# Performance work log

Hardware: AMD Instinct MI355X
Metric: run time of the kernel (lower is better)

The kernel has to match this reference:

```python
import jax, jax.numpy as jnp
import numpy as np

N, H, C, K, D = 16384, 16, 192, 43, 2
SIGMA = 1.0   # radius == sigma in Block
BN_EPS = 1e-5


def setup_inputs() -> dict:
    key = jax.random.key(0)
    ks = jax.random.split(key, 8)
    coord = jax.random.uniform(ks[0], (N, 3), dtype=jnp.float32)
    feat = jax.random.normal(ks[1], (N, C), dtype=jnp.float32)
    ref_idx = jax.random.randint(ks[2], (N, H), 0, N)
    # kernel point dispositions, within radius
    kp = jax.random.normal(ks[3], (K, 3), dtype=jnp.float32) * (0.3 * SIGMA)
    W1 = jax.random.normal(ks[4], (D, C, C), dtype=jnp.float32) / np.sqrt(C)
    Wk = jax.random.normal(ks[5], (D, K, C), dtype=jnp.float32) / np.sqrt(K * H)
    W3 = jax.random.normal(ks[6], (D, C, C), dtype=jnp.float32) / np.sqrt(C)
    ones = jnp.ones((D, C), jnp.float32)
    zeros = jnp.zeros((D, C), jnp.float32)
    return {
        "coord": coord, "feat": feat, "ref_idx": ref_idx, "kp": kp,
        "W1": W1, "Wk": Wk, "W3": W3,
        "g1": ones, "b1": zeros, "g2": ones, "b2": zeros, "g3": ones, "b3": zeros,
    }


def _bn(x, g, b):
    # PointBatchNorm on [N, C]: batch statistics over the point axis
    m = jnp.mean(x, axis=0)
    v = jnp.var(x, axis=0)
    return (x - m) * jax.lax.rsqrt(v + BN_EPS) * g + b


def reference(coord, feat, ref_idx, kp, W1, Wk, W3, g1, b1, g2, b2, g3, b3):
    # --- KP influence, shared across blocks (same coords / neighbor table) ---
    nb = coord[ref_idx] - coord[:, None, :]                       # [N,H,3] relative neighbor coords
    d2 = (jnp.sum(nb * nb, -1)[..., None]
          + jnp.sum(kp * kp, -1)[None, None, :]
          - 2.0 * jnp.einsum('nhd,kd->nhk', nb, kp))              # [N,H,K]
    d = jnp.sqrt(jnp.maximum(d2, 0.0))
    infl = jnp.maximum(1.0 - d / SIGMA, 0.0)                      # linear influence [N,H,K]

    relu = jax.nn.relu
    depth = W1.shape[0]
    for i in range(depth):
        identity = feat
        h = relu(_bn(feat @ W1[i], g1[i], b1[i]))                 # fc1 + BN + ReLU
        # KPConvD: depthwise kernel-point conv
        A = jnp.einsum('nhk,kc->nhc', infl, Wk[i])                # influence-projected depthwise weights
        h = jnp.einsum('nhc,nhc->nc', h[ref_idx], A)              # gather + weighted aggregate
        h = relu(_bn(h, g2[i], b2[i]))
        h = _bn(h @ W3[i], g3[i], b3[i])                          # fc3 + BN
        feat = relu(identity + h)                                 # skip + ReLU
    return feat
```

## Files before the change

### kernel.cpp

```cpp
#include <hip/hip_runtime.h>

#define N_PTS 16384
#define NH 16
#define NC 192
#define NK 43
#define ND 2
#define BN_EPS 1e-5f
#define NB 16
#define STSTRIDE (NB * 384)

typedef __attribute__((ext_vector_type(8))) short bf16x8;
typedef __attribute__((ext_vector_type(4))) float f32x4;

static __device__ __forceinline__ short f2bf(float f) {
    union { float f; unsigned u; } x; x.f = f;
    unsigned r = x.u + (0x7fffu + ((x.u >> 16) & 1u));
    return (short)(r >> 16);
}
static __device__ __forceinline__ float bf2f(short s) {
    union { unsigned u; float f; } x; x.u = ((unsigned)(unsigned short)s) << 16;
    return x.f;
}

static __device__ __forceinline__ void bank_sum(const float* __restrict__ acc, int c,
                                                float& s, float& q) {
    s = 0.f; q = 0.f;
#pragma unroll
    for (int k = 0; k < NB; ++k) {
        s += acc[k * 384 + c];
        q += acc[k * 384 + 192 + c];
    }
}

__global__ __launch_bounds__(64) void k_wfrag(const float* __restrict__ W1,
                                              const float* __restrict__ Wk,
                                              const float* __restrict__ W3,
                                              short* __restrict__ Wb,
                                              float* __restrict__ stacc) {
    for (int z = blockIdx.x * 64 + threadIdx.x; z < 6 * STSTRIDE; z += 336 * 64)
        stacc[z] = 0.f;

    int b = blockIdx.x;
    int d = b / 168, r = b % 168;
    const float* src; short* dst; int kb, Ks, tile;
    if (r < 72)      { src = W1 + d * NC * NC; dst = Wb + d * 86016;         kb = 6; Ks = NC; tile = r; }
    else if (r < 96) { src = Wk + d * NK * NC; dst = Wb + d * 86016 + 36864; kb = 2; Ks = NK; tile = r - 72; }
    else             { src = W3 + d * NC * NC; dst = Wb + d * 86016 + 49152; kb = 6; Ks = NC; tile = r - 96; }
    int nt = tile / kb, ks = tile % kb;
    int lane = threadIdx.x, quad = lane >> 4, cl = lane & 15;
    bf16x8 vv;
#pragma unroll
    for (int j = 0; j < 8; ++j) {
        int k = ks * 32 + quad * 8 + j;
        vv[j] = (k < Ks) ? f2bf(src[k * NC + nt * 16 + cl]) : (short)0;
    }
    *(bf16x8*)(dst + ((nt * kb + ks) * 64 + lane) * 8) = vv;
}

__global__ __launch_bounds__(256, 1) void k_gemm1(const float* __restrict__ feat,
                                                  const short* __restrict__ T2prev,
                                                  const float* __restrict__ st3acc,
                                                  const float* __restrict__ g3,
                                                  const float* __restrict__ b3,
                                                  short* __restrict__ X1,
                                                  const short* __restrict__ W1b,
                                                  short* __restrict__ T,
                                                  float* __restrict__ st1acc) {
    __shared__ float red[4][384];
    __shared__ float pa_s[192], ps_s[192];
    const int tid = threadIdx.x;
    const int wave = tid >> 6, lane = tid & 63;
    const int quad = lane >> 4, cl = lane & 15;
    const int r0 = blockIdx.x * 64 + wave * 16;
    const int row = r0 + cl;

    if (T2prev) {
        if (tid < 192) {
            float s, q; bank_sum(st3acc, tid, s, q);
            float m = s * (1.f / N_PTS);
            float v = q * (1.f / N_PTS) - m * m;
            float a = rsqrtf(v + BN_EPS) * g3[tid];
            pa_s[tid] = a;
            ps_s[tid] = b3[tid] - m * a;
        }
        __syncthreads();
    }

    float4 fa[6][2];
    bf16x8 t2v[6];
#pragma unroll
    for (int ks = 0; ks < 6; ++ks) {
        const float* ap = feat + row * NC + ks * 32 + quad * 8;
        fa[ks][0] = *(const float4*)ap;
        fa[ks][1] = *(const float4*)(ap + 4);
    }
    if (T2prev) {
#pragma unroll
        for (int ks = 0; ks < 6; ++ks)
            t2v[ks] = *(const bf16x8*)(T2prev + row * NC + ks * 32 + quad * 8);
    }

    f32x4 acc[12];
#pragma unroll
    for (int nt = 0; nt < 12; ++nt) acc[nt] = (f32x4){0.f, 0.f, 0.f, 0.f};

#pragma unroll
    for (int ks = 0; ks < 6; ++ks) {
        const int k0 = ks * 32 + quad * 8;
        float x[8] = {fa[ks][0].x, fa[ks][0].y, fa[ks][0].z, fa[ks][0].w,
                      fa[ks][1].x, fa[ks][1].y, fa[ks][1].z, fa[ks][1].w};
        if (T2prev) {
#pragma unroll
            for (int j = 0; j < 8; ++j)
                x[j] = fmaxf(x[j] + fmaf(pa_s[k0 + j], bf2f(t2v[ks][j]), ps_s[k0 + j]), 0.f);
        }
        bf16x8 af;
#pragma unroll
        for (int j = 0; j < 8; ++j) af[j] = f2bf(x[j]);
        if (T2prev) *(bf16x8*)(X1 + row * NC + k0) = af;
#pragma unroll
        for (int nt = 0; nt < 12; ++nt) {
            bf16x8 bf = *(const bf16x8*)(W1b + ((nt * 6 + ks) * 64 + lane) * 8);
            acc[nt] = __builtin_amdgcn_mfma_f32_16x16x32_bf16(af, bf, acc[nt], 0, 0, 0);
        }
    }
#pragma unroll
    for (int nt = 0; nt < 12; ++nt) {
        int c = nt * 16 + cl;
        float s = 0.f, sq = 0.f;
#pragma unroll
        for (int r = 0; r < 4; ++r) {
            float v = acc[nt][r];
            T[(r0 + quad * 4 + r) * NC + c] = f2bf(v);
            s += v; sq = fmaf(v, v, sq);
        }
        s += __shfl_xor(s, 16); s += __shfl_xor(s, 32);
        sq += __shfl_xor(sq, 16); sq += __shfl_xor(sq, 32);
        if (quad == 0) { red[wave][c] = s; red[wave][192 + c] = sq; }
    }
    __syncthreads();
    {
        float* dst = st1acc + (blockIdx.x & (NB - 1)) * 384;
        for (int t = tid; t < 384; t += 256)
            atomicAdd(&dst[t], red[0][t] + red[1][t] + red[2][t] + red[3][t]);
    }
}

__global__ __launch_bounds__(512) void k_kpconv(const float* __restrict__ coord,
                                                const int* __restrict__ ridx,
                                                const float* __restrict__ kp,
                                                const short* __restrict__ Wkb,
                                                const short* __restrict__ T,
                                                const float* __restrict__ st1acc,
                                                const float* __restrict__ g1,
                                                const float* __restrict__ b1,
                                                short* __restrict__ U,
                                                float* __restrict__ st2acc) {
    __shared__ __align__(16) short wk_s[12288];
    __shared__ __align__(16) float4 kp_s[64];
    __shared__ float a1s[192], s1s[192];
    __shared__ float red[8][384];

    const int tid = threadIdx.x;
    {
        const float4* src = (const float4*)Wkb;
        float4* dst = (float4*)wk_s;
        for (int j = tid; j < 1536; j += 512) dst[j] = src[j];
        if (tid < 64) {
            bool ok = tid < NK;
            float x = ok ? kp[tid * 3 + 0] : 1e9f;
            float y = ok ? kp[tid * 3 + 1] : 1e9f;
            float z = ok ? kp[tid * 3 + 2] : 1e9f;
            kp_s[tid] = (float4){x, y, z, fmaf(x, x, fmaf(y, y, z * z))};
        }
        if (tid < 192) {
            float s, q; bank_sum(st1acc, tid, s, q);
            float m = s * (1.f / N_PTS);
            float v = q * (1.f / N_PTS) - m * m;
            float a = rsqrtf(v + BN_EPS) * g1[tid];
            a1s[tid] = a;
            s1s[tid] = b1[tid] - m * a;
        }
    }
    __syncthreads();

    const int wave = tid >> 6, lane = tid & 63;
    const int quad = lane >> 4, cl = lane & 15;
    const int n = blockIdx.x * 8 + wave;

    int idh = 0; float nbx = 0.f, nby = 0.f, nbz = 0.f;
    if (lane < NH) {
        idh = ridx[n * NH + lane];
        float cx = coord[n * 3 + 0], cy = coord[n * 3 + 1], cz = coord[n * 3 + 2];
        nbx = coord[idh * 3 + 0] - cx;
        nby = coord[idh * 3 + 1] - cy;
        nbz = coord[idh * 3 + 2] - cz;
    }
    const float nx = __shfl(nbx, cl), ny = __shfl(nby, cl), nz = __shfl(nbz, cl);
    int rowb[4];
#pragma unroll
    for (int r = 0; r < 4; ++r) rowb[r] = __shfl(idh, quad * 4 + r) * NC;

    unsigned short xv[12][4];
    const unsigned short* Tu = (const unsigned short*)T;
#pragma unroll
    for (int nt = 0; nt < 12; ++nt)
#pragma unroll
        for (int r = 0; r < 4; ++r)
            xv[nt][r] = Tu[rowb[r] + nt * 16 + cl];

    const float nb2 = fmaf(nx, nx, fmaf(ny, ny, nz * nz));
    const float m2x = -2.f * nx, m2y = -2.f * ny, m2z = -2.f * nz;
    bf16x8 af[2];
#pragma unroll
    for (int ks = 0; ks < 2; ++ks) {
#pragma unroll
        for (int j = 0; j < 8; ++j) {
            int k = ks * 32 + quad * 8 + j;
            float4 kpv = kp_s[k];
            float t = nb2 + kpv.w;
            t = fmaf(m2x, kpv.x, t);
            t = fmaf(m2y, kpv.y, t);
            t = fmaf(m2z, kpv.z, t);
            float d = sqrtf(fmaxf(t, 0.f));
            af[ks][j] = f2bf(fmaxf(1.f - d, 0.f));
        }
    }

    f32x4 acc[12];
#pragma unroll
    for (int nt = 0; nt < 12; ++nt) {
        bf16x8 b0 = *(const bf16x8*)(wk_s + ((nt * 2 + 0) * 64 + lane) * 8);
        bf16x8 b1v = *(const bf16x8*)(wk_s + ((nt * 2 + 1) * 64 + lane) * 8);
        f32x4 z = (f32x4){0.f, 0.f, 0.f, 0.f};
        z = __builtin_amdgcn_mfma_f32_16x16x32_bf16(af[0], b0, z, 0, 0, 0);
        acc[nt] = __builtin_amdgcn_mfma_f32_16x16x32_bf16(af[1], b1v, z, 0, 0, 0);
    }

#pragma unroll
    for (int nt = 0; nt < 12; ++nt) {
        const float a1c = a1s[nt * 16 + cl], s1c = s1s[nt * 16 + cl];
        float u = 0.f;
#pragma unroll
        for (int r = 0; r < 4; ++r) {
            float t = bf2f((short)xv[nt][r]);
            float x = fmaxf(fmaf(a1c, t, s1c), 0.f);
            u = fmaf(acc[nt][r], x, u);
        }
        u += __shfl_xor(u, 16);
        u += __shfl_xor(u, 32);
        if (quad == 0) {
            U[n * NC + nt * 16 + cl] = f2bf(u);
            red[wave][nt * 16 + cl] = u;
            red[wave][192 + nt * 16 + cl] = u * u;
        }
    }

    __syncthreads();
    if (tid < 384) {
        float S = 0.f;
#pragma unroll
        for (int w = 0; w < 8; ++w) S += red[w][tid];
        atomicAdd(&st2acc[(blockIdx.x & (NB - 1)) * 384 + tid], S);
    }
}

__global__ __launch_bounds__(256, 1) void k_gemm3(const short* __restrict__ U,
                                                  const float* __restrict__ st2acc,
                                                  const float* __restrict__ g2,
                                                  const float* __restrict__ b2,
                                                  const short* __restrict__ W3b,
                                                  short* __restrict__ T2,
                                                  float* __restrict__ st3acc) {
    __shared__ float red[4][384];
    __shared__ float a2s[192], s2s[192];
    const int tid = threadIdx.x;
    const int wave = tid >> 6, lane = tid & 63;
    const int quad = lane >> 4, cl = lane & 15;
    const int r0 = blockIdx.x * 64 + wave * 16;
    const int row = r0 + cl;

    if (tid < 192) {
        float s, q; bank_sum(st2acc, tid, s, q);
        float m = s * (1.f / N_PTS);
        float v = q * (1.f / N_PTS) - m * m;
        float a = rsqrtf(v + BN_EPS) * g2[tid];
        a2s[tid] = a;
        s2s[tid] = b2[tid] - m * a;
    }
    __syncthreads();

    bf16x8 u8v[6];
#pragma unroll
    for (int ks = 0; ks < 6; ++ks)
        u8v[ks] = *(const bf16x8*)(U + row * NC + ks * 32 + quad * 8);

    f32x4 acc[12];
#pragma unroll
    for (int nt = 0; nt < 12; ++nt) acc[nt] = (f32x4){0.f, 0.f, 0.f, 0.f};

#pragma unroll
    for (int ks = 0; ks < 6; ++ks) {
        const int k0 = ks * 32 + quad * 8;
        bf16x8 af;
#pragma unroll
        for (int j = 0; j < 8; ++j)
            af[j] = f2bf(fmaxf(fmaf(a2s[k0 + j], bf2f(u8v[ks][j]), s2s[k0 + j]), 0.f));
#pragma unroll
        for (int nt = 0; nt < 12; ++nt) {
            bf16x8 bf = *(const bf16x8*)(W3b + ((nt * 6 + ks) * 64 + lane) * 8);
            acc[nt] = __builtin_amdgcn_mfma_f32_16x16x32_bf16(af, bf, acc[nt], 0, 0, 0);
        }
    }
#pragma unroll
    for (int nt = 0; nt < 12; ++nt) {
        int c = nt * 16 + cl;
        float s = 0.f, sq = 0.f;
#pragma unroll
        for (int r = 0; r < 4; ++r) {
            float v = acc[nt][r];
            T2[(r0 + quad * 4 + r) * NC + c] = f2bf(v);
            s += v; sq = fmaf(v, v, sq);
        }
        s += __shfl_xor(s, 16); s += __shfl_xor(s, 32);
        sq += __shfl_xor(sq, 16); sq += __shfl_xor(sq, 32);
        if (quad == 0) { red[wave][c] = s; red[wave][192 + c] = sq; }
    }
    __syncthreads();
    {
        float* dst = st3acc + (blockIdx.x & (NB - 1)) * 384;
        for (int t = tid; t < 384; t += 256)
            atomicAdd(&dst[t], red[0][t] + red[1][t] + red[2][t] + red[3][t]);
    }
}

__global__ __launch_bounds__(256) void k_final(const short* __restrict__ T2,
                                               const float* __restrict__ st3acc,
                                               const float* __restrict__ g3,
                                               const float* __restrict__ b3,
                                               const short* __restrict__ X1,
                                               float* __restrict__ out) {
    __shared__ float a3s[192], s3s[192];
    if (threadIdx.x < 192) {
        float s, q; bank_sum(st3acc, threadIdx.x, s, q);
        float m = s * (1.f / N_PTS);
        float v = q * (1.f / N_PTS) - m * m;
        float a = rsqrtf(v + BN_EPS) * g3[threadIdx.x];
        a3s[threadIdx.x] = a;
        s3s[threadIdx.x] = b3[threadIdx.x] - m * a;
    }
    __syncthreads();

    const int i = blockIdx.x * 256 + threadIdx.x;
    const int c0 = (i * 8) % 192;
    bf16x8 t2 = *(const bf16x8*)(T2 + (long)i * 8);
    bf16x8 x1 = *(const bf16x8*)(X1 + (long)i * 8);
    float o[8];
#pragma unroll
    for (int j = 0; j < 8; ++j)
        o[j] = fmaxf(bf2f(x1[j]) + fmaf(a3s[c0 + j], bf2f(t2[j]), s3s[c0 + j]), 0.f);
    *(float4*)(out + (long)i * 8)     = (float4){o[0], o[1], o[2], o[3]};
    *(float4*)(out + (long)i * 8 + 4) = (float4){o[4], o[5], o[6], o[7]};
}

extern "C" void kernel_launch(void* const* d_in, const int* in_sizes, int n_in,
                              void* d_out, int out_size, void* d_ws, size_t ws_size,
                              hipStream_t stream) {
    const float* coord = (const float*)d_in[0];
    const float* feat  = (const float*)d_in[1];
    const int*   ridx  = (const int*)d_in[2];
    const float* kp    = (const float*)d_in[3];
    const float* W1    = (const float*)d_in[4];
    const float* Wk    = (const float*)d_in[5];
    const float* W3    = (const float*)d_in[6];
    const float* g1    = (const float*)d_in[7];
    const float* b1    = (const float*)d_in[8];
    const float* g2    = (const float*)d_in[9];
    const float* b2    = (const float*)d_in[10];
    const float* g3    = (const float*)d_in[11];
    const float* b3    = (const float*)d_in[12];
    float* out = (float*)d_out;

    float* stacc = (float*)d_ws;
    short* X1 = (short*)(stacc + 6 * STSTRIDE);
    short* T  = X1 + N_PTS * NC;
    short* U  = T + N_PTS * NC;
    short* T2 = U + N_PTS * NC;
    short* Wb = T2 + N_PTS * NC;

    k_wfrag<<<336, 64, 0, stream>>>(W1, Wk, W3, Wb, stacc);

    for (int d = 0; d < ND; ++d) {
        const short* W1b = Wb + d * 86016;
        const short* Wkb = W1b + 36864;
        const short* W3b = W1b + 49152;
        float* st1acc = stacc + (d * 3 + 0) * STSTRIDE;
        float* st2acc = stacc + (d * 3 + 1) * STSTRIDE;
        float* st3acc = stacc + (d * 3 + 2) * STSTRIDE;

        k_gemm1<<<256, 256, 0, stream>>>(feat,
                                         d ? T2 : (short*)nullptr,
                                         stacc + 2 * STSTRIDE,
                                         g3, b3,
                                         X1, W1b, T, st1acc);
        k_kpconv<<<N_PTS / 8, 512, 0, stream>>>(coord, ridx, kp, Wkb, T,
                                                st1acc, g1 + d * NC, b1 + d * NC,
                                                U, st2acc);
        k_gemm3<<<256, 256, 0, stream>>>(U, st2acc, g2 + d * NC, b2 + d * NC,
                                         W3b, T2, st3acc);
    }
    k_final<<<N_PTS * NC / 8 / 256, 256, 0, stream>>>(T2, stacc + 5 * STSTRIDE,
                                                      g3 + NC, b3 + NC, X1, out);
}
```

Before: 227.1 us.

## Split GEMM column tiles across waves and launch four times more blocks

The fc1 and fc3 GEMM kernels now give each block 16 rows, with its four waves splitting the 12 output column tiles (3 each), in place of 64 rows per block with every wave computing all 12 tiles. The grid grows from 256 to 1024 blocks and launch bounds allow 4 blocks per CU, so the point-wise GEMMs spread across more CUs with fewer accumulator registers per wave. The shared-memory reduction and barrier for the BN statistics are removed in favour of direct per-wave atomics. The cost is redundant loading and conversion of the A rows by all four waves, plus many more atomic adds on the 16 stat banks.

```diff
diff --git a/kernel.cpp b/kernel.cpp
--- a/kernel.cpp
+++ b/kernel.cpp
@@ -57,7 +57,7 @@
     *(bf16x8*)(dst + ((nt * kb + ks) * 64 + lane) * 8) = vv;
 }
 
-__global__ __launch_bounds__(256, 1) void k_gemm1(const float* __restrict__ feat,
+__global__ __launch_bounds__(256, 4) void k_gemm1(const float* __restrict__ feat,
                                                   const short* __restrict__ T2prev,
                                                   const float* __restrict__ st3acc,
                                                   const float* __restrict__ g3,
@@ -66,12 +66,11 @@
                                                   const short* __restrict__ W1b,
                                                   short* __restrict__ T,
                                                   float* __restrict__ st1acc) {
-    __shared__ float red[4][384];
     __shared__ float pa_s[192], ps_s[192];
     const int tid = threadIdx.x;
-    const int wave = tid >> 6, lane = tid & 63;
+    const int cq = tid >> 6, lane = tid & 63;
     const int quad = lane >> 4, cl = lane & 15;
-    const int r0 = blockIdx.x * 64 + wave * 16;
+    const int r0 = blockIdx.x * 16;
     const int row = r0 + cl;
 
     if (T2prev) {
@@ -100,9 +99,9 @@
             t2v[ks] = *(const bf16x8*)(T2prev + row * NC + ks * 32 + quad * 8);
     }
 
-    f32x4 acc[12];
-#pragma unroll
-    for (int nt = 0; nt < 12; ++nt) acc[nt] = (f32x4){0.f, 0.f, 0.f, 0.f};
+    f32x4 acc[3];
+#pragma unroll
+    for (int nt = 0; nt < 3; ++nt) acc[nt] = (f32x4){0.f, 0.f, 0.f, 0.f};
 
 #pragma unroll
     for (int ks = 0; ks < 6; ++ks) {
@@ -117,16 +116,17 @@
         bf16x8 af;
 #pragma unroll
         for (int j = 0; j < 8; ++j) af[j] = f2bf(x[j]);
-        if (T2prev) *(bf16x8*)(X1 + row * NC + k0) = af;
-#pragma unroll
-        for (int nt = 0; nt < 12; ++nt) {
-            bf16x8 bf = *(const bf16x8*)(W1b + ((nt * 6 + ks) * 64 + lane) * 8);
+        if (T2prev && cq == 0) *(bf16x8*)(X1 + row * NC + k0) = af;
+#pragma unroll
+        for (int nt = 0; nt < 3; ++nt) {
+            const int ntg = cq * 3 + nt;
+            bf16x8 bf = *(const bf16x8*)(W1b + ((ntg * 6 + ks) * 64 + lane) * 8);
             acc[nt] = __builtin_amdgcn_mfma_f32_16x16x32_bf16(af, bf, acc[nt], 0, 0, 0);
         }
     }
 #pragma unroll
-    for (int nt = 0; nt < 12; ++nt) {
-        int c = nt * 16 + cl;
+    for (int nt = 0; nt < 3; ++nt) {
+        int c = (cq * 3 + nt) * 16 + cl;
         float s = 0.f, sq = 0.f;
 #pragma unroll
         for (int r = 0; r < 4; ++r) {
@@ -136,13 +136,11 @@
         }
         s += __shfl_xor(s, 16); s += __shfl_xor(s, 32);
         sq += __shfl_xor(sq, 16); sq += __shfl_xor(sq, 32);
-        if (quad == 0) { red[wave][c] = s; red[wave][192 + c] = sq; }
-    }
-    __syncthreads();
-    {
-        float* dst = st1acc + (blockIdx.x & (NB - 1)) * 384;
-        for (int t = tid; t < 384; t += 256)
-            atomicAdd(&dst[t], red[0][t] + red[1][t] + red[2][t] + red[3][t]);
+        if (quad == 0) {
+            float* dst = st1acc + (blockIdx.x & (NB - 1)) * 384;
+            atomicAdd(&dst[c], s);
+            atomicAdd(&dst[192 + c], sq);
+        }
     }
 }
 
@@ -265,19 +263,18 @@
     }
 }
 
-__global__ __launch_bounds__(256, 1) void k_gemm3(const short* __restrict__ U,
+__global__ __launch_bounds__(256, 4) void k_gemm3(const short* __restrict__ U,
                                                   const float* __restrict__ st2acc,
                                                   const float* __restrict__ g2,
                                                   const float* __restrict__ b2,
                                                   const short* __restrict__ W3b,
                                                   short* __restrict__ T2,
                                                   float* __restrict__ st3acc) {
-    __shared__ float red[4][384];
     __shared__ float a2s[192], s2s[192];
     const int tid = threadIdx.x;
-    const int wave = tid >> 6, lane = tid & 63;
+    const int cq = tid >> 6, lane = tid & 63;
     const int quad = lane >> 4, cl = lane & 15;
-    const int r0 = blockIdx.x * 64 + wave * 16;
+    const int r0 = blockIdx.x * 16;
     const int row = r0 + cl;
 
     if (tid < 192) {
@@ -295,9 +292,9 @@
     for (int ks = 0; ks < 6; ++ks)
         u8v[ks] = *(const bf16x8*)(U + row * NC + ks * 32 + quad * 8);
 
-    f32x4 acc[12];
-#pragma unroll
-    for (int nt = 0; nt < 12; ++nt) acc[nt] = (f32x4){0.f, 0.f, 0.f, 0.f};
+    f32x4 acc[3];
+#pragma unroll
+    for (int nt = 0; nt < 3; ++nt) acc[nt] = (f32x4){0.f, 0.f, 0.f, 0.f};
 
 #pragma unroll
     for (int ks = 0; ks < 6; ++ks) {
@@ -307,14 +304,15 @@
         for (int j = 0; j < 8; ++j)
             af[j] = f2bf(fmaxf(fmaf(a2s[k0 + j], bf2f(u8v[ks][j]), s2s[k0 + j]), 0.f));
 #pragma unroll
-        for (int nt = 0; nt < 12; ++nt) {
-            bf16x8 bf = *(const bf16x8*)(W3b + ((nt * 6 + ks) * 64 + lane) * 8);
+        for (int nt = 0; nt < 3; ++nt) {
+            const int ntg = cq * 3 + nt;
+            bf16x8 bf = *(const bf16x8*)(W3b + ((ntg * 6 + ks) * 64 + lane) * 8);
             acc[nt] = __builtin_amdgcn_mfma_f32_16x16x32_bf16(af, bf, acc[nt], 0, 0, 0);
         }
     }
 #pragma unroll
-    for (int nt = 0; nt < 12; ++nt) {
-        int c = nt * 16 + cl;
+    for (int nt = 0; nt < 3; ++nt) {
+        int c = (cq * 3 + nt) * 16 + cl;
         float s = 0.f, sq = 0.f;
 #pragma unroll
         for (int r = 0; r < 4; ++r) {
@@ -324,13 +322,11 @@
         }
         s += __shfl_xor(s, 16); s += __shfl_xor(s, 32);
         sq += __shfl_xor(sq, 16); sq += __shfl_xor(sq, 32);
-        if (quad == 0) { red[wave][c] = s; red[wave][192 + c] = sq; }
-    }
-    __syncthreads();
-    {
-        float* dst = st3acc + (blockIdx.x & (NB - 1)) * 384;
-        for (int t = tid; t < 384; t += 256)
-            atomicAdd(&dst[t], red[0][t] + red[1][t] + red[2][t] + red[3][t]);
+        if (quad == 0) {
+            float* dst = st3acc + (blockIdx.x & (NB - 1)) * 384;
+            atomicAdd(&dst[c], s);
+            atomicAdd(&dst[192 + c], sq);
+        }
     }
 }
 
@@ -398,16 +394,16 @@
         float* st2acc = stacc + (d * 3 + 1) * STSTRIDE;
         float* st3acc = stacc + (d * 3 + 2) * STSTRIDE;
 
-        k_gemm1<<<256, 256, 0, stream>>>(feat,
-                                         d ? T2 : (short*)nullptr,
-                                         stacc + 2 * STSTRIDE,
-                                         g3, b3,
-                                         X1, W1b, T, st1acc);
+        k_gemm1<<<N_PTS / 16, 256, 0, stream>>>(feat,
+                                                d ? T2 : (short*)nullptr,
+                                                stacc + 2 * STSTRIDE,
+                                                g3, b3,
+                                                X1, W1b, T, st1acc);
         k_kpconv<<<N_PTS / 8, 512, 0, stream>>>(coord, ridx, kp, Wkb, T,
                                                 st1acc, g1 + d * NC, b1 + d * NC,
                                                 U, st2acc);
-        k_gemm3<<<256, 256, 0, stream>>>(U, st2acc, g2 + d * NC, b2 + d * NC,
-                                         W3b, T2, st3acc);
+        k_gemm3<<<N_PTS / 16, 256, 0, stream>>>(U, st2acc, g2 + d * NC, b2 + d * NC,
+                                                W3b, T2, st3acc);
     }
     k_final<<<N_PTS * NC / 8 / 256, 256, 0, stream>>>(T2, stacc + 5 * STSTRIDE,
                                                       g3 + NC, b3 + NC, X1, out);
```

Result: faster. 218.5 us (-3.8%).
